# Performance work log

Measured on AMD Instinct MI355X. Metric: run time of the kernel, lower is better.

## Reference

```python
import jax, jax.numpy as jnp
import numpy as np

A = 9               # anchors per location (3 scales x 3 ratios)
STRIDE = 32         # backbone stride 16 * conv1 stride 2
PRE_NMS = 2000      # boxes kept before NMS
POST_NMS = 300      # rois kept after NMS
NMS_THRESH = 0.7
MIN_SIZE = 16.0
NEG = jnp.float32(-1e30)


def _generate_anchors(base_size=16, ratios=(0.5, 1.0, 2.0), scales=(8, 16, 32)):
    xc = yc = 0.5 * (base_size - 1)
    size = float(base_size * base_size)
    anchors = []
    for r in ratios:
        ws = np.round(np.sqrt(size / r))
        hs = np.round(ws * r)
        for s in scales:
            w, h = ws * s, hs * s
            anchors.append([xc - 0.5 * (w - 1), yc - 0.5 * (h - 1),
                            xc + 0.5 * (w - 1), yc + 0.5 * (h - 1)])
    return np.array(anchors, dtype=np.float32)  # [A,4]


def _conv(x, w, b, stride, pad):
    y = jax.lax.conv_general_dilated(
        x, w, (stride, stride), ((pad, pad), (pad, pad)),
        dimension_numbers=('NCHW', 'OIHW', 'NCHW'))
    return y + b[None, :, None, None]


def _iou_matrix(boxes):
    x1, y1, x2, y2 = boxes[:, 0], boxes[:, 1], boxes[:, 2], boxes[:, 3]
    area = (x2 - x1 + 1.0) * (y2 - y1 + 1.0)
    iw = jnp.maximum(0.0, jnp.minimum(x2[:, None], x2[None, :]) - jnp.maximum(x1[:, None], x1[None, :]) + 1.0)
    ih = jnp.maximum(0.0, jnp.minimum(y2[:, None], y2[None, :]) - jnp.maximum(y1[:, None], y1[None, :]) + 1.0)
    inter = iw * ih
    return inter / (area[:, None] + area[None, :] - inter)


def _nms_single(boxes, scores):
    # boxes [K,4] sorted by score desc; scores [K] (NEG = filtered out)
    K = boxes.shape[0]
    iou = _iou_matrix(boxes)
    prio = jnp.arange(K, 0, -1)

    def step(valid, _):
        any_valid = jnp.any(valid)
        pick = jnp.argmax(jnp.where(valid, prio, 0))
        new_valid = valid & (iou[pick] <= NMS_THRESH)
        return new_valid, (pick, any_valid)

    valid0 = scores > NEG * 0.5
    _, (picks, flags) = jax.lax.scan(step, valid0, None, length=POST_NMS)
    sel = boxes[picks] * flags[:, None].astype(boxes.dtype)
    return sel, jnp.sum(flags.astype(jnp.int32))


def _proposal(deltas, scores):
    B, _, H, W = deltas.shape
    im_h, im_w = float(H * STRIDE), float(W * STRIDE)
    anchors = jnp.asarray(_generate_anchors())  # [A,4]
    sx = (jnp.arange(W) * STRIDE).astype(jnp.float32)
    sy = (jnp.arange(H) * STRIDE).astype(jnp.float32)
    gx, gy = jnp.meshgrid(sx, sy)  # [H,W] each
    shift = jnp.stack([gx, gy, gx, gy], axis=-1)  # [H,W,4]
    anc = (shift[:, :, None, :] + anchors[None, None, :, :]).reshape(-1, 4)  # [H*W*A,4]

    d = deltas.reshape(B, A, 4, H, W).transpose(0, 3, 4, 1, 2).reshape(B, -1, 4)  # [B,N,4]
    s = scores[:, A:].transpose(0, 2, 3, 1).reshape(B, -1)  # fg scores [B,N]

    ws = anc[:, 2] - anc[:, 0] + 1.0
    hs = anc[:, 3] - anc[:, 1] + 1.0
    cx = anc[:, 0] + 0.5 * ws
    cy = anc[:, 1] + 0.5 * hs
    pcx = d[:, :, 0] * ws + cx
    pcy = d[:, :, 1] * hs + cy
    pw = jnp.exp(d[:, :, 2]) * ws
    ph = jnp.exp(d[:, :, 3]) * hs
    boxes = jnp.stack([pcx - 0.5 * pw, pcy - 0.5 * ph,
                       pcx + 0.5 * pw, pcy + 0.5 * ph], axis=-1)  # [B,N,4]
    lim = jnp.array([im_w - 1, im_h - 1, im_w - 1, im_h - 1], jnp.float32)
    boxes = jnp.minimum(jnp.maximum(boxes, 0.0), lim)

    bw = boxes[..., 2] - boxes[..., 0] + 1.0
    bh = boxes[..., 3] - boxes[..., 1] + 1.0
    s = jnp.where((bw >= MIN_SIZE) & (bh >= MIN_SIZE), s, NEG)

    top_s, idx = jax.lax.top_k(s, PRE_NMS)  # sorted desc
    top_b = jnp.take_along_axis(boxes, idx[:, :, None], axis=1)  # [B,PRE,4]

    sel, num = jax.vmap(_nms_single)(top_b, top_s)  # [B,POST,4], [B]
    bidx = jnp.broadcast_to(jnp.arange(B, dtype=sel.dtype)[:, None, None], (B, POST_NMS, 1))
    rois = jnp.concatenate([bidx, sel], axis=-1)  # [B,POST,5]
    return rois, num


def setup_inputs() -> dict:
    key = jax.random.key(0)
    k = jax.random.split(key, 4)
    x = jax.random.normal(k[0], (4, 512, 96, 160), jnp.float32)
    w1 = jax.random.normal(k[1], (512, 512, 3, 3), jnp.float32) * 0.02
    b1 = jnp.zeros((512,), jnp.float32)
    w_bbox = jax.random.normal(k[2], (36, 512, 1, 1), jnp.float32) * 0.02
    b_bbox = jnp.zeros((36,), jnp.float32)
    w_cls = jax.random.normal(k[3], (18, 512, 3, 3), jnp.float32) * 0.02
    b_cls = jnp.zeros((18,), jnp.float32)
    return dict(x=x, w1=w1, b1=b1, w_bbox=w_bbox, b_bbox=b_bbox, w_cls=w_cls, b_cls=b_cls)


def reference(x, w1, b1, w_bbox, b_bbox, w_cls, b_cls):
    feat = _conv(x, w1, b1, 2, 1)           # [B,512,H/2,W/2]
    deltas = _conv(feat, w_bbox, b_bbox, 1, 0)  # [B,36,h,w]
    cls = _conv(feat, w_cls, b_cls, 1, 1)       # [B,18,h,w]
    return _proposal(deltas, cls)
```

## Files before the change

kernel.cpp:

```cpp
#include <hip/hip_runtime.h>
#include <stdint.h>

typedef unsigned long long u64;
typedef unsigned int u32;
typedef float v2f __attribute__((ext_vector_type(2)));

__constant__ float c_aw[9] = {184.f,368.f,736.f,128.f,256.f,512.f, 88.f,176.f,352.f};
__constant__ float c_ah[9] = { 96.f,192.f,384.f,128.f,256.f,512.f,176.f,352.f,704.f};

__global__ __launch_bounds__(256) void transpose_k(const float* __restrict__ w1,
                                                   float* __restrict__ wt2) {
  int e = blockIdx.x * 256 + threadIdx.x;
  int m = e & 7;
  int t = e >> 3;
  int k = t % 9;
  int r = t / 9;
  int ci = r & 511;
  int g = r >> 9;
  wt2[e] = w1[(size_t)(g * 8 + m) * 4608 + ci * 9 + k];
}

__global__ __launch_bounds__(256, 3) void conv1_k(const float* __restrict__ x,
                                                  const float* __restrict__ wt2,
                                                  const float* __restrict__ b1,
                                                  float* __restrict__ feat) {
  __shared__ float xs[8 * 9 * 164];
  const int tid = threadIdx.x;
  const int lane = tid & 63;
  const int wv = __builtin_amdgcn_readfirstlane(tid >> 6);
  const int owg = lane & 15;
  const int ohl = lane >> 4;
  const int n = blockIdx.z;
  const int gg = blockIdx.x * 4 + wv;
  const int oh0 = blockIdx.y * 4;
  const int ih_base = 2 * oh0 - 1;

  int soff[6], loff[6];
  float okf[6];
  bool act[6];
#pragma unroll
  for (int it = 0; it < 6; ++it) {
    int e2 = tid + 256 * it;
    act[it] = (e2 < 1449);
    int e = act[it] ? e2 : 0;
    int ih = e / 161;
    int c = e - ih * 161;
    int gih = ih_base + ih;
    int giw = c - 1;
    bool ok = act[it] && ((unsigned)gih < 96u) && ((unsigned)giw < 160u);
    soff[it] = min(max(gih, 0), 95) * 160 + min(max(giw, 0), 159);
    loff[it] = ih * 164 + c;
    okf[it] = ok ? 1.f : 0.f;
  }

  v2f acc[4][5];
#pragma unroll
  for (int q = 0; q < 4; ++q)
#pragma unroll
    for (int j = 0; j < 5; ++j) acc[q][j] = (v2f){0.f, 0.f};

  const float* xb = x + (size_t)n * 512 * 96 * 160;
  const float* wgb = wt2 + (size_t)gg * 512 * 72;

  float r[6][8];
#pragma unroll
  for (int it = 0; it < 6; ++it)
#pragma unroll
    for (int ci = 0; ci < 8; ++ci)
      r[it][ci] = xb[(size_t)ci * 15360 + soff[it]];

  for (int c0 = 0; c0 < 512; c0 += 8) {
    __syncthreads();
#pragma unroll
    for (int it = 0; it < 6; ++it) {
      if (act[it]) {
        const float m_ = okf[it];
#pragma unroll
        for (int ci = 0; ci < 8; ++ci)
          xs[loff[it] + ci * 1476] = m_ * r[it][ci];
      }
    }
    __syncthreads();
    if (c0 + 8 < 512) {
      const float* xn = xb + (size_t)(c0 + 8) * 15360;
#pragma unroll
      for (int it = 0; it < 6; ++it)
#pragma unroll
        for (int ci = 0; ci < 8; ++ci)
          r[it][ci] = xn[(size_t)ci * 15360 + soff[it]];
    }

    for (int ci = 0; ci < 8; ++ci) {
      const float* wp = wgb + (size_t)(c0 + ci) * 72;
      const float* xrow = &xs[(ci * 9 + 2 * ohl) * 164 + owg * 10];
#pragma unroll
      for (int kh = 0; kh < 3; ++kh) {
        float xv[12];
        const float* xr = xrow + kh * 164;
#pragma unroll
        for (int t2 = 0; t2 < 6; ++t2) {
          float2 tt = *(const float2*)(xr + 2 * t2);
          xv[2 * t2] = tt.x; xv[2 * t2 + 1] = tt.y;
        }
#pragma unroll
        for (int kw = 0; kw < 3; ++kw) {
          const v2f* wk2 = (const v2f*)(wp + (kh * 3 + kw) * 8);
          const v2f w0 = wk2[0], w1 = wk2[1], w2 = wk2[2], w3 = wk2[3];
#pragma unroll
          for (int j = 0; j < 5; ++j) {
            const float xj = xv[kw + 2 * j];
            const v2f xx = {xj, xj};
            acc[0][j] = __builtin_elementwise_fma(w0, xx, acc[0][j]);
            acc[1][j] = __builtin_elementwise_fma(w1, xx, acc[1][j]);
            acc[2][j] = __builtin_elementwise_fma(w2, xx, acc[2][j]);
            acc[3][j] = __builtin_elementwise_fma(w3, xx, acc[3][j]);
          }
        }
      }
    }
  }
  const int oh = oh0 + ohl;
  const int owb = owg * 5;
#pragma unroll
  for (int q = 0; q < 4; ++q) {
    const int co = gg * 8 + 2 * q;
    const float bx = b1[co], by = b1[co + 1];
    float* opx = &feat[(((size_t)n * 512 + co) * 48 + oh) * 80 + owb];
    float* opy = opx + 3840;
#pragma unroll
    for (int j = 0; j < 5; ++j) {
      opx[j] = acc[q][j].x + bx;
      opy[j] = acc[q][j].y + by;
    }
  }
}

__global__ __launch_bounds__(256) void heads_k(const float* __restrict__ feat,
                                               const float* __restrict__ wb,
                                               const float* __restrict__ bb,
                                               const float* __restrict__ wcg,
                                               const float* __restrict__ bc,
                                               float* __restrict__ deltas,
                                               float* __restrict__ s) {
  __shared__ float smem[5328];
  const int tid = threadIdx.x;

  if (blockIdx.x < 120) {
    float* fs  = smem;
    float* wsb = smem + 2048;
    const int blk = blockIdx.x;
    const int b = blk / 30;
    const int pos0 = (blk % 30) * 128;
    const int pl = tid >> 1, cg = tid & 1;
    const int cbase = cg * 18;
    const float* fb = feat + (size_t)b * 512 * 3840;

    int fso[8];
#pragma unroll
    for (int p = 0; p < 8; ++p) {
      int e = tid + 256 * p;
      fso[p] = (e >> 7) * 3840 + pos0 + (e & 127);
    }
    int wso[3]; bool wact[3];
#pragma unroll
    for (int p = 0; p < 3; ++p) {
      int e = tid + 256 * p;
      wact[p] = (e < 576);
      int ee = wact[p] ? e : 0;
      wso[p] = (ee % 36) * 512 + (ee / 36);
    }
    float acc[18];
#pragma unroll
    for (int j = 0; j < 18; ++j) acc[j] = 0.f;

    float rf[8], rw[3];
#pragma unroll
    for (int p = 0; p < 8; ++p) rf[p] = fb[fso[p]];
#pragma unroll
    for (int p = 0; p < 3; ++p) rw[p] = wb[wso[p]];

    for (int t = 0; t < 32; ++t) {
      __syncthreads();
#pragma unroll
      for (int p = 0; p < 8; ++p) fs[tid + 256 * p] = rf[p];
#pragma unroll
      for (int p = 0; p < 3; ++p)
        if (wact[p]) wsb[tid + 256 * p] = rw[p];
      __syncthreads();
      if (t < 31) {
        const float* fn = fb + (size_t)(t + 1) * 16 * 3840;
        const float* wn = wb + (t + 1) * 16;
#pragma unroll
        for (int p = 0; p < 8; ++p) rf[p] = fn[fso[p]];
#pragma unroll
        for (int p = 0; p < 3; ++p) rw[p] = wn[wso[p]];
      }
      for (int ci = 0; ci < 16; ++ci) {
        float xv = fs[ci * 128 + pl];
#pragma unroll
        for (int j = 0; j < 18; ++j) acc[j] += xv * wsb[ci * 36 + cbase + j];
      }
    }
    size_t o = ((size_t)b * 3840 + pos0 + pl) * 36 + cbase;
#pragma unroll
    for (int j = 0; j < 18; ++j) deltas[o + j] = acc[j] + bb[cbase + j];
  } else {
    float* fsf = smem;
    float* wcf = smem + 4032;
    const int bid2 = blockIdx.x - 120;
    const int oh = bid2 % 48;
    const int b = bid2 / 48;
    const int pos = tid % 80;
    const int cg = tid / 80;
    const float* fb = feat + (size_t)b * 512 * 3840;

    int fso3[16], lof3[16];
    float fok3[16];
    bool fact3[16];
#pragma unroll
    for (int p = 0; p < 16; ++p) {
      int e = tid + 256 * p;
      fact3[p] = (e < 3936);
      int ee = fact3[p] ? e : 0;
      int ci = ee / 246;
      int r = ee - ci * 246;
      int ihl = r / 82;
      int iw = r - ihl * 82 - 1;
      int gih = oh - 1 + ihl;
      bool ok = fact3[p] && ((unsigned)gih < 48u) && ((unsigned)iw < 80u);
      fso3[p] = ci * 3840 + min(max(gih, 0), 47) * 80 + min(max(iw, 0), 79);
      lof3[p] = ci * 252 + ihl * 84 + iw + 1;
      fok3[p] = ok ? 1.f : 0.f;
    }
    int wso3[6]; bool wact3[6];
#pragma unroll
    for (int p = 0; p < 6; ++p) {
      int e = tid + 256 * p;
      wact3[p] = (e < 1296);
      int ee = wact3[p] ? e : 0;
      int ci = ee / 81;
      int r = ee - ci * 81;
      int co = r / 9;
      int k = r - co * 9;
      wso3[p] = ((size_t)(9 + co) * 512 + ci) * 9 + k;
    }
    float acc[3] = {0.f, 0.f, 0.f};

    float rf3[16], rw3[6];
#pragma unroll
    for (int p = 0; p < 16; ++p) rf3[p] = fb[fso3[p]];
#pragma unroll
    for (int p = 0; p < 6; ++p) rw3[p] = wcg[wso3[p]];

    for (int t = 0; t < 32; ++t) {
      __syncthreads();
#pragma unroll
      for (int p = 0; p < 16; ++p)
        if (fact3[p]) fsf[lof3[p]] = fok3[p] * rf3[p];
#pragma unroll
      for (int p = 0; p < 6; ++p)
        if (wact3[p]) wcf[tid + 256 * p] = rw3[p];
      __syncthreads();
      if (t < 31) {
        const float* fn = fb + (size_t)(t + 1) * 16 * 3840;
        const float* wn = wcg + (t + 1) * 144;
#pragma unroll
        for (int p = 0; p < 16; ++p) rf3[p] = fn[fso3[p]];
#pragma unroll
        for (int p = 0; p < 6; ++p) rw3[p] = wn[wso3[p]];
      }
      if (cg < 3) {
        const int cb = cg * 3;
        for (int ci = 0; ci < 16; ++ci) {
#pragma unroll
          for (int kh = 0; kh < 3; ++kh) {
#pragma unroll
            for (int kw = 0; kw < 3; ++kw) {
              float xv = fsf[ci * 252 + kh * 84 + pos + kw];
              acc[0] += xv * wcf[ci * 81 + (cb + 0) * 9 + kh * 3 + kw];
              acc[1] += xv * wcf[ci * 81 + (cb + 1) * 9 + kh * 3 + kw];
              acc[2] += xv * wcf[ci * 81 + (cb + 2) * 9 + kh * 3 + kw];
            }
          }
        }
      }
    }
    if (cg < 3) {
      const int cb = cg * 3;
      size_t o = (size_t)b * 34560 + ((size_t)oh * 80 + pos) * 9 + cb;
#pragma unroll
      for (int j = 0; j < 3; ++j) s[o + j] = acc[j] + bc[9 + cb + j];
    }
  }
}

__global__ __launch_bounds__(256) void decode_k(const float* __restrict__ deltas,
                                                const float* __restrict__ s,
                                                float* __restrict__ boxes,
                                                u64* __restrict__ keys) {
  const int g = blockIdx.x * 256 + threadIdx.x;
  const int b = g / 34560;
  const int i = g - b * 34560;
  const int pos = i / 9;
  const int a = i - pos * 9;
  const int h = pos / 80;
  const int w = pos - h * 80;
  const float gx = (float)(w * 32);
  const float gy = (float)(h * 32);
  const float aw = c_aw[a], ah = c_ah[a];
  const float x1a = 7.5f - 0.5f * (aw - 1.f);
  const float y1a = 7.5f - 0.5f * (ah - 1.f);
  const float ws_ = aw, hs_ = ah;
  const float cx = (gx + x1a) + 0.5f * ws_;
  const float cy = (gy + y1a) + 0.5f * hs_;

  const float* dp = &deltas[((size_t)b * 3840 + pos) * 36 + a * 4];
  const float d0 = dp[0], d1 = dp[1], d2 = dp[2], d3 = dp[3];
  const float pcx = __fadd_rn(__fmul_rn(d0, ws_), cx);
  const float pcy = __fadd_rn(__fmul_rn(d1, hs_), cy);
  const float pw = __fmul_rn(expf(d2), ws_);
  const float ph = __fmul_rn(expf(d3), hs_);
  float bx1 = __fsub_rn(pcx, __fmul_rn(0.5f, pw));
  float by1 = __fsub_rn(pcy, __fmul_rn(0.5f, ph));
  float bx2 = __fadd_rn(pcx, __fmul_rn(0.5f, pw));
  float by2 = __fadd_rn(pcy, __fmul_rn(0.5f, ph));
  bx1 = fminf(fmaxf(bx1, 0.f), 2559.f);
  by1 = fminf(fmaxf(by1, 0.f), 1535.f);
  bx2 = fminf(fmaxf(bx2, 0.f), 2559.f);
  by2 = fminf(fmaxf(by2, 0.f), 1535.f);
  const float bw = __fadd_rn(__fsub_rn(bx2, bx1), 1.f);
  const float bh = __fadd_rn(__fsub_rn(by2, by1), 1.f);
  float sc = s[g];
  if (!(bw >= 16.f && bh >= 16.f)) sc = -1e30f;

  float4 bo;
  bo.x = bx1; bo.y = by1; bo.z = bx2; bo.w = by2;
  *(float4*)&boxes[(size_t)g * 4] = bo;

  u32 sb = __float_as_uint(sc);
  u32 ou = (sb & 0x80000000u) ? ~sb : (sb | 0x80000000u);
  keys[g] = ((u64)ou << 32) | (u32)(~(u32)i);
}

__global__ __launch_bounds__(1024) void selcomp_k(const u64* __restrict__ keys,
                                                  u64* __restrict__ sel) {
  __shared__ u32 h[16384];
  __shared__ u64 cand[6144];
  __shared__ u32 wsum[16], wsuf[16];
  __shared__ int s_bin, s_above, s_main, s_nc;
  const int b = blockIdx.x;
  const int tid = threadIdx.x;
  const int lane = tid & 63;
  const int wv = tid >> 6;
  const u64* kb = keys + (size_t)b * 34560;

#pragma unroll
  for (int q = 0; q < 16; ++q) h[tid + 1024 * q] = 0;
  __syncthreads();
  for (int i = tid; i < 34560; i += 1024)
    atomicAdd(&h[(u32)(kb[i] >> 50)], 1u);
  __syncthreads();

  const int i0 = tid * 16;
  u32 myb[16];
  u32 tsum = 0;
#pragma unroll
  for (int q = 0; q < 16; ++q) { myb[q] = h[i0 + q]; tsum += myb[q]; }
  u32 sfx = tsum;
#pragma unroll
  for (int off = 1; off < 64; off <<= 1) {
    u32 o = __shfl_down(sfx, off, 64);
    if (lane + off < 64) sfx += o;
  }
  if (lane == 0) wsum[wv] = sfx;
  __syncthreads();
  if (tid < 16) {
    u32 v = wsum[tid];
#pragma unroll
    for (int off = 1; off < 16; off <<= 1) {
      u32 o = __shfl_down(v, off, 64);
      if (tid + off < 16) v += o;
    }
    wsuf[tid] = v;
  }
  __syncthreads();
  const u32 wave_base = (wv < 15) ? wsuf[wv + 1] : 0u;
  u32 accu = wave_base + (sfx - tsum);
#pragma unroll
  for (int q = 15; q >= 0; --q) { accu += myb[q]; h[i0 + q] = accu; }
  __syncthreads();

#pragma unroll
  for (int q = 0; q < 16; ++q) {
    int bn = i0 + q;
    u32 Si = h[bn];
    u32 Sn = (bn < 16383) ? h[bn + 1] : 0u;
    if ((int)Si >= 2000 && (int)Sn < 2000) { s_bin = bn; s_above = (int)Sn; }
  }
  if (tid == 0) { s_main = 0; s_nc = 0; }
  __syncthreads();
  const u32 B = (u32)s_bin;
  const int above = s_above;
  const int need = 2000 - above;

  for (int i = tid; i < 34560; i += 1024) {
    u64 k = kb[i];
    u32 t14 = (u32)(k >> 50);
    if (t14 > B) {
      int p = atomicAdd(&s_main, 1);
      sel[(size_t)b * 2048 + p] = k;
    } else if (t14 == B) {
      int p = atomicAdd(&s_nc, 1);
      if (p < 6144) cand[p] = k;
    }
  }
  __syncthreads();
  const int nc = min(s_nc, 6144);
  for (int c = tid; c < nc; c += 1024) {
    u64 kc = cand[c];
    int rnk = 0;
    for (int j = 0; j < nc; ++j) rnk += (cand[j] > kc) ? 1 : 0;
    if (rnk < need) sel[(size_t)b * 2048 + above + rnk] = kc;
  }
}

__global__ __launch_bounds__(1024) void sort_k(const u64* __restrict__ sel,
                                               const float* __restrict__ boxes,
                                               float* __restrict__ sx1, float* __restrict__ sy1,
                                               float* __restrict__ sx2, float* __restrict__ sy2,
                                               float* __restrict__ sar, u32* __restrict__ sval) {
  __shared__ u64 K[2048];
  __shared__ unsigned char val[2048];
  const int b = blockIdx.x;
  const int tid = threadIdx.x;

  for (int i = tid; i < 2048; i += 1024)
    K[i] = (i < 2000) ? sel[(size_t)b * 2048 + i] : 0ull;
  __syncthreads();
  for (int k2 = 2; k2 <= 2048; k2 <<= 1) {
    for (int j = k2 >> 1; j > 0; j >>= 1) {
      for (int i = tid; i < 2048; i += 1024) {
        int l = i ^ j;
        if (l > i) {
          u64 a = K[i], c = K[l];
          bool up = ((i & k2) == 0);
          if (up ? (a < c) : (a > c)) { K[i] = c; K[l] = a; }
        }
      }
      __syncthreads();
    }
  }
  for (int i = tid; i < 2048; i += 1024) {
    float x1v = 0.f, y1v = 0.f, x2v = 0.f, y2v = 0.f, arv = 1.f;
    unsigned char vb = 0;
    if (i < 2000) {
      u64 key = K[i];
      u32 ou = (u32)(key >> 32);
      int idx = (int)(~(u32)key);
      u32 sb = (ou & 0x80000000u) ? (ou & 0x7FFFFFFFu) : ~ou;
      float sc = __uint_as_float(sb);
      const float4 bo = *(const float4*)&boxes[((size_t)b * 34560 + idx) * 4];
      x1v = bo.x; y1v = bo.y; x2v = bo.z; y2v = bo.w;
      arv = __fmul_rn(__fadd_rn(__fsub_rn(bo.z, bo.x), 1.f),
                      __fadd_rn(__fsub_rn(bo.w, bo.y), 1.f));
      vb = (sc > -5e29f) ? 1 : 0;
    }
    size_t o = (size_t)b * 2048 + i;
    sx1[o] = x1v; sy1[o] = y1v; sx2[o] = x2v; sy2[o] = y2v; sar[o] = arv;
    val[i] = vb;
  }
  __syncthreads();
  if (tid < 64) {
    u32 w = 0;
#pragma unroll
    for (int q = 0; q < 32; ++q)
      w |= (val[tid * 32 + q] ? 1u : 0u) << q;
    sval[b * 64 + tid] = w;
  }
}

__global__ __launch_bounds__(256) void iou_k(const float* __restrict__ sx1, const float* __restrict__ sy1,
                                             const float* __restrict__ sx2, const float* __restrict__ sy2,
                                             const float* __restrict__ sar,
                                             u64* __restrict__ supp) {
  __shared__ float lx1[2048], ly1[2048], lx2[2048], ly2[2048], lar[2048];
  const int b = blockIdx.y;
  const int r0 = blockIdx.x * 128;
  const int tid = threadIdx.x;
  const int lane = tid & 63;
  const int wq = tid >> 6;
  const size_t base = (size_t)b * 2048;

  for (int i = tid; i < 2048; i += 256) {
    lx1[i] = sx1[base + i]; ly1[i] = sy1[base + i];
    lx2[i] = sx2[base + i]; ly2[i] = sy2[base + i];
    lar[i] = sar[base + i];
  }
  __syncthreads();

  for (int i = r0; i < r0 + 128; ++i) {
    const float px1 = lx1[i], py1 = ly1[i], px2 = lx2[i], py2 = ly2[i], pa = lar[i];
    u64* row = supp + ((size_t)b * 2048 + i) * 32;
#pragma unroll
    for (int s2 = 0; s2 < 8; ++s2) {
      const int j = s2 * 256 + wq * 64 + lane;
      float iw = __fadd_rn(__fsub_rn(fminf(px2, lx2[j]), fmaxf(px1, lx1[j])), 1.f);
      iw = fmaxf(0.f, iw);
      float ih = __fadd_rn(__fsub_rn(fminf(py2, ly2[j]), fmaxf(py1, ly1[j])), 1.f);
      ih = fmaxf(0.f, ih);
      const float inter = __fmul_rn(iw, ih);
      const float denom = __fsub_rn(__fadd_rn(pa, lar[j]), inter);
      const float iou = __fdiv_rn(inter, denom);
      const u64 bits = __ballot(iou > 0.7f);
      if (lane == 0) row[s2 * 4 + wq] = bits;
    }
  }
}

__global__ __launch_bounds__(64) void scan_k(const u32* __restrict__ sval,
                                             const u64* __restrict__ supp,
                                             const float* __restrict__ sx1, const float* __restrict__ sy1,
                                             const float* __restrict__ sx2, const float* __restrict__ sy2,
                                             float* __restrict__ out) {
  const int b = blockIdx.x;
  const int lane = threadIdx.x;
  u32 v = sval[b * 64 + lane];
  const size_t base = (size_t)b * 2048;

  int cnt = 0;
  for (int t = 0; t < 300; ++t) {
    u64 m = __ballot(v != 0);
    if (m == 0) break;
    const int f = __ffsll(m) - 1;
    const u32 fw = __shfl(v, f, 64);
    const int p = f * 32 + (__ffs(fw) - 1);
    if (lane == 0) {
      float* row = out + ((size_t)b * 300 + t) * 5;
      row[0] = (float)b;
      row[1] = sx1[base + p]; row[2] = sy1[base + p];
      row[3] = sx2[base + p]; row[4] = sy2[base + p];
    }
    cnt = t + 1;
    const u64 w8 = supp[(base + p) * 32 + (lane >> 1)];
    const u32 sup = (lane & 1) ? (u32)(w8 >> 32) : (u32)w8;
    v &= ~sup;
  }
  for (int t2 = cnt + lane; t2 < 300; t2 += 64) {
    float* row = out + ((size_t)b * 300 + t2) * 5;
    row[0] = (float)b; row[1] = 0.f; row[2] = 0.f; row[3] = 0.f; row[4] = 0.f;
  }
  if (lane == 0) out[6000 + b] = (float)cnt;
}

extern "C" void kernel_launch(void* const* d_in, const int* in_sizes, int n_in,
                              void* d_out, int out_size, void* d_ws, size_t ws_size,
                              hipStream_t stream) {
  const float* x  = (const float*)d_in[0];
  const float* w1 = (const float*)d_in[1];
  const float* b1 = (const float*)d_in[2];
  const float* wb = (const float*)d_in[3];
  const float* bb = (const float*)d_in[4];
  const float* wc = (const float*)d_in[5];
  const float* bc = (const float*)d_in[6];
  float* out = (float*)d_out;
  char* ws = (char*)d_ws;

  float* feat   = (float*)(ws + 0);
  float* wt2    = (float*)(ws + 31457280);
  float* deltas = (float*)(ws + 40894464);
  float* s      = (float*)(ws + 43106304);
  float* boxes  = (float*)(ws + 43659264);
  u64*   keys   = (u64*)  (ws + 45871104);
  u64*   sel    = (u64*)  (ws + 46977088);
  float* sx1    = (float*)(ws + 47042624);
  float* sy1    = (float*)(ws + 47075392);
  float* sx2    = (float*)(ws + 47108160);
  float* sy2    = (float*)(ws + 47140928);
  float* sar    = (float*)(ws + 47173696);
  u32*   sval   = (u32*)  (ws + 47206464);
  u64*   supp   = (u64*)  (ws + 47207488);

  hipLaunchKernelGGL(transpose_k, dim3(9216), dim3(256), 0, stream, w1, wt2);
  hipLaunchKernelGGL(conv1_k, dim3(16, 12, 4), dim3(256), 0, stream, x, wt2, b1, feat);
  hipLaunchKernelGGL(heads_k, dim3(312), dim3(256), 0, stream, feat, wb, bb, wc, bc, deltas, s);
  hipLaunchKernelGGL(decode_k, dim3(540), dim3(256), 0, stream, deltas, s, boxes, keys);
  hipLaunchKernelGGL(selcomp_k, dim3(4), dim3(1024), 0, stream, keys, sel);
  hipLaunchKernelGGL(sort_k, dim3(4), dim3(1024), 0, stream, sel, boxes, sx1, sy1, sx2, sy2, sar, sval);
  hipLaunchKernelGGL(iou_k, dim3(16, 4), dim3(256), 0, stream, sx1, sy1, sx2, sy2, sar, supp);
  hipLaunchKernelGGL(scan_k, dim3(4), dim3(64), 0, stream, sval, supp, sx1, sy1, sx2, sy2, out);
}
```

Baseline: 1.378 ms.

## Fuse top-k selection with rank sort, tile weight transpose, force packed FMA

The separate bitonic sort kernel is removed. Selection now places the above-threshold keys in shared memory, ranks them by all-pairs counting, and writes the sorted box arrays and valid-bit words directly, which saves a launch and the global round trip through sel. The weight transpose now uses a shared-memory tile per output group with coalesced reads, running on 64 blocks instead of 9216. The conv inner loop uses inline-asm v_pk_fma_f32 to guarantee packed FMA issue. The O(n^2) rank count over up to 2000 mains runs on only 4 blocks, and the asm may restrict compiler scheduling.

Result: slower. 1.622 ms (+17.6%).

```diff
diff --git a/kernel.cpp b/kernel.cpp
--- a/kernel.cpp
+++ b/kernel.cpp
@@ -5,19 +5,32 @@
 typedef unsigned int u32;
 typedef float v2f __attribute__((ext_vector_type(2)));
 
+static __device__ __forceinline__ void pk_fma(v2f& d, v2f a, v2f b) {
+  asm("v_pk_fma_f32 %0, %1, %2, %0" : "+v"(d) : "v"(a), "v"(b));
+}
+
 __constant__ float c_aw[9] = {184.f,368.f,736.f,128.f,256.f,512.f, 88.f,176.f,352.f};
 __constant__ float c_ah[9] = { 96.f,192.f,384.f,128.f,256.f,512.f,176.f,352.f,704.f};
 
 __global__ __launch_bounds__(256) void transpose_k(const float* __restrict__ w1,
                                                    float* __restrict__ wt2) {
-  int e = blockIdx.x * 256 + threadIdx.x;
-  int m = e & 7;
-  int t = e >> 3;
-  int k = t % 9;
-  int r = t / 9;
-  int ci = r & 511;
-  int g = r >> 9;
-  wt2[e] = w1[(size_t)(g * 8 + m) * 4608 + ci * 9 + k];
+  __shared__ float t[8][577];
+  const int g = blockIdx.x;
+  const int tid = threadIdx.x;
+  for (int ch = 0; ch < 8; ++ch) {
+    for (int e = tid; e < 8 * 576; e += 256) {
+      int m = e / 576, q = e - m * 576;
+      t[m][q] = w1[(size_t)(g * 8 + m) * 4608 + ch * 576 + q];
+    }
+    __syncthreads();
+    float* outp = wt2 + (size_t)g * 512 * 72 + ch * 4608;
+    for (int e2 = tid; e2 < 4608; e2 += 256) {
+      int m = e2 & 7;
+      int r = e2 >> 3;
+      outp[e2] = t[m][r];
+    }
+    __syncthreads();
+  }
 }
 
 __global__ __launch_bounds__(256, 3) void conv1_k(const float* __restrict__ x,
@@ -110,10 +123,10 @@
           for (int j = 0; j < 5; ++j) {
             const float xj = xv[kw + 2 * j];
             const v2f xx = {xj, xj};
-            acc[0][j] = __builtin_elementwise_fma(w0, xx, acc[0][j]);
-            acc[1][j] = __builtin_elementwise_fma(w1, xx, acc[1][j]);
-            acc[2][j] = __builtin_elementwise_fma(w2, xx, acc[2][j]);
-            acc[3][j] = __builtin_elementwise_fma(w3, xx, acc[3][j]);
+            pk_fma(acc[0][j], w0, xx);
+            pk_fma(acc[1][j], w1, xx);
+            pk_fma(acc[2][j], w2, xx);
+            pk_fma(acc[3][j], w3, xx);
           }
         }
       }
@@ -343,9 +356,14 @@
 }
 
 __global__ __launch_bounds__(1024) void selcomp_k(const u64* __restrict__ keys,
-                                                  u64* __restrict__ sel) {
+                                                  const float* __restrict__ boxes,
+                                                  float* __restrict__ sx1, float* __restrict__ sy1,
+                                                  float* __restrict__ sx2, float* __restrict__ sy2,
+                                                  float* __restrict__ sar, u32* __restrict__ sval) {
   __shared__ u32 h[16384];
   __shared__ u64 cand[6144];
+  __shared__ u64 mains[2048];
+  __shared__ unsigned char vbyte[2048];
   __shared__ u32 wsum[16], wsuf[16];
   __shared__ int s_bin, s_above, s_main, s_nc;
   const int b = blockIdx.x;
@@ -408,53 +426,36 @@
     u32 t14 = (u32)(k >> 50);
     if (t14 > B) {
       int p = atomicAdd(&s_main, 1);
-      sel[(size_t)b * 2048 + p] = k;
+      mains[p] = k;
     } else if (t14 == B) {
       int p = atomicAdd(&s_nc, 1);
       if (p < 6144) cand[p] = k;
     }
   }
   __syncthreads();
+  u64* sorted = (u64*)h;
+  const int mcnt = s_main;
   const int nc = min(s_nc, 6144);
+  for (int c = tid; c < mcnt; c += 1024) {
+    u64 kc = mains[c];
+    int rnk = 0;
+    for (int j = 0; j < mcnt; ++j) rnk += (mains[j] > kc) ? 1 : 0;
+    sorted[rnk] = kc;
+  }
   for (int c = tid; c < nc; c += 1024) {
     u64 kc = cand[c];
     int rnk = 0;
     for (int j = 0; j < nc; ++j) rnk += (cand[j] > kc) ? 1 : 0;
-    if (rnk < need) sel[(size_t)b * 2048 + above + rnk] = kc;
-  }
-}
-
-__global__ __launch_bounds__(1024) void sort_k(const u64* __restrict__ sel,
-                                               const float* __restrict__ boxes,
-                                               float* __restrict__ sx1, float* __restrict__ sy1,
-                                               float* __restrict__ sx2, float* __restrict__ sy2,
-                                               float* __restrict__ sar, u32* __restrict__ sval) {
-  __shared__ u64 K[2048];
-  __shared__ unsigned char val[2048];
-  const int b = blockIdx.x;
-  const int tid = threadIdx.x;
-
-  for (int i = tid; i < 2048; i += 1024)
-    K[i] = (i < 2000) ? sel[(size_t)b * 2048 + i] : 0ull;
-  __syncthreads();
-  for (int k2 = 2; k2 <= 2048; k2 <<= 1) {
-    for (int j = k2 >> 1; j > 0; j >>= 1) {
-      for (int i = tid; i < 2048; i += 1024) {
-        int l = i ^ j;
-        if (l > i) {
-          u64 a = K[i], c = K[l];
-          bool up = ((i & k2) == 0);
-          if (up ? (a < c) : (a > c)) { K[i] = c; K[l] = a; }
-        }
-      }
-      __syncthreads();
-    }
-  }
+    if (rnk < need) sorted[above + rnk] = kc;
+  }
+  for (int i = 2000 + tid; i < 2048; i += 1024) sorted[i] = 0ull;
+  __syncthreads();
+
   for (int i = tid; i < 2048; i += 1024) {
     float x1v = 0.f, y1v = 0.f, x2v = 0.f, y2v = 0.f, arv = 1.f;
     unsigned char vb = 0;
     if (i < 2000) {
-      u64 key = K[i];
+      u64 key = sorted[i];
       u32 ou = (u32)(key >> 32);
       int idx = (int)(~(u32)key);
       u32 sb = (ou & 0x80000000u) ? (ou & 0x7FFFFFFFu) : ~ou;
@@ -467,14 +468,14 @@
     }
     size_t o = (size_t)b * 2048 + i;
     sx1[o] = x1v; sy1[o] = y1v; sx2[o] = x2v; sy2[o] = y2v; sar[o] = arv;
-    val[i] = vb;
+    vbyte[i] = vb;
   }
   __syncthreads();
   if (tid < 64) {
     u32 w = 0;
 #pragma unroll
     for (int q = 0; q < 32; ++q)
-      w |= (val[tid * 32 + q] ? 1u : 0u) << q;
+      w |= (vbyte[tid * 32 + q] ? 1u : 0u) << q;
     sval[b * 64 + tid] = w;
   }
 }
@@ -571,7 +572,6 @@
   float* s      = (float*)(ws + 43106304);
   float* boxes  = (float*)(ws + 43659264);
   u64*   keys   = (u64*)  (ws + 45871104);
-  u64*   sel    = (u64*)  (ws + 46977088);
   float* sx1    = (float*)(ws + 47042624);
   float* sy1    = (float*)(ws + 47075392);
   float* sx2    = (float*)(ws + 47108160);
@@ -580,12 +580,12 @@
   u32*   sval   = (u32*)  (ws + 47206464);
   u64*   supp   = (u64*)  (ws + 47207488);
 
-  hipLaunchKernelGGL(transpose_k, dim3(9216), dim3(256), 0, stream, w1, wt2);
+  hipLaunchKernelGGL(transpose_k, dim3(64), dim3(256), 0, stream, w1, wt2);
   hipLaunchKernelGGL(conv1_k, dim3(16, 12, 4), dim3(256), 0, stream, x, wt2, b1, feat);
   hipLaunchKernelGGL(heads_k, dim3(312), dim3(256), 0, stream, feat, wb, bb, wc, bc, deltas, s);
   hipLaunchKernelGGL(decode_k, dim3(540), dim3(256), 0, stream, deltas, s, boxes, keys);
-  hipLaunchKernelGGL(selcomp_k, dim3(4), dim3(1024), 0, stream, keys, sel);
-  hipLaunchKernelGGL(sort_k, dim3(4), dim3(1024), 0, stream, sel, boxes, sx1, sy1, sx2, sy2, sar, sval);
+  hipLaunchKernelGGL(selcomp_k, dim3(4), dim3(1024), 0, stream, keys, boxes,
+                     sx1, sy1, sx2, sy2, sar, sval);
   hipLaunchKernelGGL(iou_k, dim3(16, 4), dim3(256), 0, stream, sx1, sy1, sx2, sy2, sar, supp);
   hipLaunchKernelGGL(scan_k, dim3(4), dim3(64), 0, stream, sval, supp, sx1, sy1, sx2, sy2, out);
 }
```
